# Kernel optimization log

Measured on AMD Instinct MI355X. Metric: run time of the kernel, lower is better.

Reference implementation:

```python
import jax, jax.numpy as jnp
import numpy as np
from jax import lax

CORRKS = 7
EPS_CORR = 1e-6
EPS_IN = 1e-5
FLOW_SCALE = 1.0


def _gauss_kernel2d():
    # kornia get_gaussian_kernel1d(7, 1.5), separable -> outer product
    x = np.arange(7, dtype=np.float32) - 3.0
    g = np.exp(-(x ** 2) / (2.0 * 1.5 ** 2))
    g = g / g.sum()
    return jnp.asarray(np.outer(g, g), dtype=jnp.float32)  # [7,7]


def conv2d(x, w, b=None, padding=1, dilation=1, groups=1):
    y = lax.conv_general_dilated(
        x, w, window_strides=(1, 1),
        padding=[(padding, padding), (padding, padding)],
        rhs_dilation=(dilation, dilation),
        dimension_numbers=("NCHW", "OIHW", "NCHW"),
        feature_group_count=groups)
    if b is not None:
        y = y + b[None, :, None, None]
    return y


def gaussian_blur(x):
    # replicate padding then depthwise 7x7 gaussian conv
    c = x.shape[1]
    k2 = _gauss_kernel2d()
    w = jnp.broadcast_to(k2[None, None], (c, 1, 7, 7))
    xp = jnp.pad(x, ((0, 0), (0, 0), (3, 3), (3, 3)), mode="edge")
    return conv2d(xp, w, padding=0, groups=c)


def instance_norm(x, gamma, beta):
    mu = x.mean(axis=(2, 3), keepdims=True)
    var = x.var(axis=(2, 3), keepdims=True)
    xn = (x - mu) * lax.rsqrt(var + EPS_IN)
    return xn * gamma[None, :, None, None] + beta[None, :, None, None]


def lrelu(x):
    return jnp.where(x >= 0, x, 0.2 * x)


def nan0(x):
    return jnp.nan_to_num(x, nan=0.0, posinf=0.0, neginf=0.0)


def setup_inputs() -> dict:
    key = jax.random.key(0)
    ks = jax.random.split(key, 20)
    b, c, h, w = 4, 64, 256, 256

    def rn(k, shape, scale):
        return jax.random.normal(k, shape, dtype=jnp.float32) * scale

    d = {}
    d["feat1"] = rn(ks[0], (b, c, h, w), 1.0)
    d["feat2"] = rn(ks[1], (b, c, h, w), 1.0)
    # preprocessor: Conv(c, c, 3, pad=1), bias, no norm/act
    d["pre_w"] = rn(ks[2], (c, c, 3, 3), 0.05)
    d["pre_b"] = jnp.zeros((c,), jnp.float32)
    # featcompressor layer1: Conv(2c,2c,3), IN affine + LeakyReLU (no bias)
    d["fc1_w"] = rn(ks[3], (2 * c, 2 * c, 3, 3), 0.05)
    d["fc1_g"] = jnp.ones((2 * c,), jnp.float32)
    d["fc1_be"] = jnp.zeros((2 * c,), jnp.float32)
    # featcompressor layer2: Conv(2c,c,3), bias, no norm/act
    d["fc2_w"] = rn(ks[4], (c, 2 * c, 3, 3), 0.05)
    d["fc2_b"] = jnp.zeros((c,), jnp.float32)
    # estimator: (c+49)->64 d1, 64->32 d2, 32->16 d4; IN + LeakyReLU, no bias
    d["e1_w"] = rn(ks[5], (64, c + CORRKS * CORRKS, 3, 3), 0.05)
    d["e1_g"] = jnp.ones((64,), jnp.float32)
    d["e1_be"] = jnp.zeros((64,), jnp.float32)
    d["e2_w"] = rn(ks[6], (32, 64, 3, 3), 0.05)
    d["e2_g"] = jnp.ones((32,), jnp.float32)
    d["e2_be"] = jnp.zeros((32,), jnp.float32)
    d["e3_w"] = rn(ks[7], (16, 32, 3, 3), 0.05)
    d["e3_g"] = jnp.ones((16,), jnp.float32)
    d["e3_be"] = jnp.zeros((16,), jnp.float32)
    # flow head (torch zero-inits; use small random so output is non-degenerate)
    d["head_w"] = rn(ks[8], (2, 16, 3, 3), 0.05)
    d["head_b"] = jnp.zeros((2,), jnp.float32)
    return d


def reference(feat1, feat2, pre_w, pre_b, fc1_w, fc1_g, fc1_be, fc2_w, fc2_b,
              e1_w, e1_g, e1_be, e2_w, e2_g, e2_be, e3_w, e3_g, e3_be,
              head_w, head_b):
    # preprocessor applied to both features (cat on batch == apply separately)
    f1 = conv2d(feat1, pre_w, pre_b, padding=1)
    f2 = conv2d(feat2, pre_w, pre_b, padding=1)

    # featcompressor
    feat = conv2d(jnp.concatenate([f1, f2], axis=1), fc1_w, padding=1)
    feat = lrelu(instance_norm(feat, fc1_g, fc1_be))
    feat = conv2d(feat, fc2_w, fc2_b, padding=1)

    # local correlation: (feat2 - shifted blurred feat1)^2 mean over channels
    b, c, h, w = f2.shape
    f1s = gaussian_blur(f1)
    pad = CORRKS // 2  # corr_dilation=1
    f1p = jnp.pad(f1s, ((0, 0), (0, 0), (pad, pad), (pad, pad)))  # zero pad (F.unfold)
    lc = jnp.stack(
        [((f2 - f1p[:, :, i:i + h, j:j + w]) ** 2).mean(axis=1)
         for i in range(CORRKS) for j in range(CORRKS)], axis=1)  # [b,49,h,w]
    lc = lc / (lc.mean(axis=(1, 2, 3), keepdims=True) + EPS_CORR)
    corr = nan0(jnp.concatenate([feat, lc], axis=1))  # [b, c+49, h, w]

    # dilated conv estimator stack
    x = lrelu(instance_norm(conv2d(corr, e1_w, padding=1, dilation=1), e1_g, e1_be))
    x = lrelu(instance_norm(conv2d(x, e2_w, padding=2, dilation=2), e2_g, e2_be))
    x = lrelu(instance_norm(conv2d(x, e3_w, padding=4, dilation=4), e3_g, e3_be))

    disp = conv2d(x, head_w, head_b, padding=1) * FLOW_SCALE
    disp = nan0(gaussian_blur(disp))
    return disp
```

## Files before the change

### kernel.cpp

```cpp
#include <hip/hip_runtime.h>
#include <hip/hip_bf16.h>


typedef __attribute__((ext_vector_type(8))) short short8;
typedef __attribute__((ext_vector_type(4))) float f32x4;
typedef _Float16 f16x8 __attribute__((ext_vector_type(8)));

__device__ __forceinline__ float s2f(short s) {
    unsigned int u = ((unsigned int)(unsigned short)s) << 16;
    float f; __builtin_memcpy(&f, &u, 4); return f;
}
__device__ __forceinline__ short f2s(float f) {
    __hip_bfloat16 h = __float2bfloat16(f);
    short s; __builtin_memcpy(&s, &h, 2); return s;
}
__device__ __forceinline__ short f2h(float f) {
    _Float16 h = (_Float16)f;
    short s; __builtin_memcpy(&s, &h, 2); return s;
}

__device__ __forceinline__ float gw(int j) {
    const float G[7] = {0.0366329f, 0.1112808f, 0.2167453f, 0.2706821f,
                        0.2167453f, 0.1112808f, 0.0366329f};
    return G[j];
}

__global__ __launch_bounds__(256) void transpose_k(const float* __restrict__ in,
                                                   short* __restrict__ out)
{
    __shared__ float t[64][65];
    const int b = blockIdx.y;
    const int px0 = blockIdx.x * 64;
    #pragma unroll
    for (int k = 0; k < 16; ++k) {
        int idx = threadIdx.x + k * 256;
        int c = idx >> 6, x = idx & 63;
        t[c][x] = in[(size_t)(b * 64 + c) * 65536 + px0 + x];
    }
    __syncthreads();
    #pragma unroll
    for (int k = 0; k < 16; ++k) {
        int idx = threadIdx.x + k * 256;
        int px = idx >> 6, c = idx & 63;
        out[(size_t)(b * 65536 + px0 + px) * 64 + c] = f2s(t[c][px]);
    }
}

__global__ __launch_bounds__(256) void repack2_k(const float* __restrict__ w,
                                                 short* __restrict__ o,
                                                 int cout, int cin, int CINP)
{
    int idx = blockIdx.x * 256 + threadIdx.x;
    int CB = CINP >> 5;
    int tot = cout * 9 * CINP;
    if (idx >= tot) return;
    int c8   = idx & 7;
    int lane = (idx >> 3) & 63;
    int rest = idx >> 9;
    int cb   = rest % CB;
    int rest2 = rest / CB;
    int tap  = rest2 % 9;
    int o16  = rest2 / 9;
    int n16 = lane & 15, q = lane >> 4;
    int oc = o16 * 16 + n16;
    int ic = cb * 32 + q * 8 + c8;
    float v = (ic < cin) ? w[(size_t)(oc * cin + ic) * 9 + tap] : 0.f;
    o[idx] = f2s(v);
}

template<int DIL, int CINP, int WX, int WY, int NOC, int G, int MODE>
__global__ __launch_bounds__(256) void convmfma_k(
    const short* __restrict__ srcA, const short* __restrict__ srcB,
    int splitK, int csA, int csB,
    const short* __restrict__ wgt, const float* __restrict__ bias,
    short* __restrict__ out, int OSTR, int OBASE, int b0,
    const float* __restrict__ xf)
{
    static_assert(WX * WY == 4, "4 waves per block");
    constexpr int PXW = G * 16;
    constexpr int PXB = PXW * WX;
    constexpr int XT  = 256 / PXB;
    constexpr int CB  = CINP / 32;
    constexpr int UQ  = CINP / 8;
    constexpr int LUQ = (UQ == 16) ? 4 : ((UQ == 8) ? 3 : 2);
    static_assert(UQ == (1 << LUQ), "UQ must be 4/8/16");
    constexpr int UPX = UQ + 1;
    constexpr int WPX = PXB + 2 * DIL;
    constexpr int NTOT = WPX * UQ;
    constexpr int NIT  = (NTOT + 255) / 256;

    __shared__ __align__(16) short lds[WPX * UPX * 8];

    const int tid  = threadIdx.x;
    const int lane = tid & 63;
    const int wave = tid >> 6;
    const int q = lane >> 4, n16 = lane & 15;
    const int wx = wave % WX, wy = wave / WX;

    constexpr int NX = XT * 256;
    const int bx = blockIdx.x;
    const int xs = (bx & 7) * (NX >> 3) + (bx >> 3);
    const int xt = xs % XT;
    const int y  = xs / XT;

    const int b  = b0 + blockIdx.z;
    const int ocWaveBase = blockIdx.y * (16 * NOC * WY) + wy * (16 * NOC);
    const int o16base = ocWaveBase >> 4;
    const int x0 = xt * PXB + wx * PXW;
    const int gxbase = xt * PXB - DIL;

    const int bC = b * CINP;
    const float sc = (MODE == 2) ? 1.f / (xf[b] * (1.f / 3211264.f) + 1e-6f) : 0.f;

    short8 stg[NIT];

    auto issue = [&](int yy) {
        const int rowbase = (b * 256 + yy) * 256;
        #pragma unroll
        for (int it = 0; it < NIT; ++it) {
            const int i = tid + it * 256;
            short8 v = {0, 0, 0, 0, 0, 0, 0, 0};
            if (i < NTOT) {
                const int pxl = i >> LUQ;
                const int u   = i & (UQ - 1);
                const int gx  = gxbase + pxl;
                if ((unsigned)gx < 256u) {
                    const int ic = u * 8;
                    const short* p = (ic < splitK)
                        ? srcA + (size_t)(rowbase + gx) * csA + ic
                        : srcB + (size_t)(rowbase + gx) * csB + (ic - splitK);
                    v = *reinterpret_cast<const short8*>(p);
                }
            }
            stg[it] = v;
        }
    };

    auto commit = [&]() {
        #pragma unroll
        for (int it = 0; it < NIT; ++it) {
            const int i = tid + it * 256;
            if (i < NTOT) {
                const int pxl = i >> LUQ;
                const int u   = i & (UQ - 1);
                short8 v = stg[it];
                if (MODE == 1) {
                    const int gx = gxbase + pxl;
                    if ((unsigned)gx < 256u) {
                        const int ic = u * 8;
                        #pragma unroll
                        for (int c = 0; c < 8; ++c) {
                            const float ka = xf[2 * (bC + ic + c)];
                            const float kb = xf[2 * (bC + ic + c) + 1];
                            float t = s2f(v[c]) * ka + kb;
                            t = fmaxf(t, 0.2f * t);
                            v[c] = f2s(t);
                        }
                    }
                } else if (MODE == 2) {
                    const int gx = gxbase + pxl;
                    const int ic = u * 8;
                    if ((unsigned)gx < 256u && ic >= splitK) {
                        #pragma unroll
                        for (int c = 0; c < 8; ++c)
                            v[c] = f2s(s2f(v[c]) * sc);
                    }
                }
                *reinterpret_cast<short8*>(&lds[(pxl * UPX + u) * 8]) = v;
            }
        }
    };

    f32x4 acc[G][NOC];
    #pragma unroll
    for (int g = 0; g < G; ++g)
        #pragma unroll
        for (int t = 0; t < NOC; ++t)
            acc[g][t] = {0.f, 0.f, 0.f, 0.f};

    {
        const int yy0 = y - DIL;
        if ((unsigned)yy0 < 256u) issue(yy0);
    }

    for (int dyi = 0; dyi < 3; ++dyi) {
        const int yy = y + (dyi - 1) * DIL;
        const bool rowok = ((unsigned)yy < 256u);
        __syncthreads();
        if (rowok) commit();
        __syncthreads();
        if (dyi < 2) {
            const int yn = y + dyi * DIL;
            if ((unsigned)yn < 256u) issue(yn);
        }
        if (!rowok) continue;

        #pragma unroll
        for (int dxi = 0; dxi < 3; ++dxi) {
            const int tap = dyi * 3 + dxi;
            #pragma unroll
            for (int cb = 0; cb < CB; ++cb) {
                short8 bfr[G];
                #pragma unroll
                for (int g = 0; g < G; ++g) {
                    const int pxl = wx * PXW + g * 16 + n16 + dxi * DIL;
                    bfr[g] = *reinterpret_cast<const short8*>(
                        &lds[(pxl * UPX + cb * 4 + q) * 8]);
                }
                #pragma unroll
                for (int t = 0; t < NOC; ++t) {
                    short8 a = *reinterpret_cast<const short8*>(
                        wgt + ((((size_t)(o16base + t) * 9 + tap) * CB + cb) * 64 + lane) * 8);
                    #pragma unroll
                    for (int g = 0; g < G; ++g)
                        acc[g][t] = __builtin_amdgcn_mfma_f32_16x16x32_bf16(
                            a, bfr[g], acc[g][t], 0, 0, 0);
                }
            }
        }
    }

    #pragma unroll
    for (int g = 0; g < G; ++g) {
        const size_t px_lin = (size_t)(b * 256 + y) * 256 + x0 + g * 16 + n16;
        #pragma unroll
        for (int t = 0; t < NOC; ++t) {
            const int oc = ocWaveBase + t * 16 + q * 4;
            f32x4 v = acc[g][t];
            if (bias) {
                v.x += bias[oc];     v.y += bias[oc + 1];
                v.z += bias[oc + 2]; v.w += bias[oc + 3];
            }
            ushort4 pk;
            pk.x = (unsigned short)f2s(v.x);
            pk.y = (unsigned short)f2s(v.y);
            pk.z = (unsigned short)f2s(v.z);
            pk.w = (unsigned short)f2s(v.w);
            *reinterpret_cast<ushort4*>(out + px_lin * OSTR + OBASE + oc) = pk;
        }
    }
}

__global__ __launch_bounds__(256) void in_stats_nhwc_k(const short* __restrict__ x,
                                                       float* __restrict__ sums,
                                                       int C, int lC)
{
    __shared__ float ls[256], lss[256];
    const int tid = threadIdx.x;
    const int b = blockIdx.y;
    const int c = tid & (C - 1);
    const int sub = tid >> lC;
    const int tpc = 256 >> lC;
    const int px0 = blockIdx.x * 512;
    float s = 0.f, ss = 0.f;
    for (int p = sub; p < 512; p += tpc) {
        float v = s2f(x[(size_t)(b * 65536 + px0 + p) * C + c]);
        s += v; ss += v * v;
    }
    ls[tid] = s; lss[tid] = ss;
    __syncthreads();
    if (tid < C) {
        float s0 = ls[tid], ss0 = lss[tid];
        for (int j = 1; j < tpc; ++j) { s0 += ls[tid + j * C]; ss0 += lss[tid + j * C]; }
        atomicAdd(sums + 2 * (b * C + tid), s0);
        atomicAdd(sums + 2 * (b * C + tid) + 1, ss0);
    }
}

__global__ __launch_bounds__(256) void in_finalize_k(const float* __restrict__ sums,
                                                     float* __restrict__ stats,
                                                     const float* __restrict__ gamma,
                                                     const float* __restrict__ beta,
                                                     int lC, int n)
{
    int i = blockIdx.x * 256 + threadIdx.x;
    if (i >= n) return;
    int c = i & ((1 << lC) - 1);
    float m = sums[2 * i] * (1.f / 65536.f);
    float var = sums[2 * i + 1] * (1.f / 65536.f) - m * m;
    if (var < 0.f) var = 0.f;
    float ka = rsqrtf(var + 1e-5f) * gamma[c];
    stats[2 * i] = ka;
    stats[2 * i + 1] = beta[c] - m * ka;
}

__global__ __launch_bounds__(256) void blur_k(const short* __restrict__ A,
                                              short* __restrict__ B1)
{
    __shared__ __align__(16) short raw[484 * 8];
    __shared__ __align__(16) float hb[352 * 12];

    const int tid  = threadIdx.x;
    const int tile = blockIdx.x >> 3;
    const int g    = blockIdx.x & 7;
    const int c0   = g * 8;
    const int tx = (tile & 15) << 4;
    const int ty = (tile >> 4) << 4;
    const int b  = blockIdx.y;

    #pragma unroll
    for (int it = 0; it < 2; ++it) {
        int i = tid + it * 256;
        if (i < 484) {
            int y = i / 22, x = i - y * 22;
            int gy = ty + y - 3, gx = tx + x - 3;
            gy = gy < 0 ? 0 : (gy > 255 ? 255 : gy);
            gx = gx < 0 ? 0 : (gx > 255 ? 255 : gx);
            *reinterpret_cast<short8*>(&raw[i * 8]) =
                *reinterpret_cast<const short8*>(
                    &A[(size_t)((b << 16) + (gy << 8) + gx) * 128 + c0]);
        }
    }
    __syncthreads();

    #pragma unroll
    for (int it = 0; it < 2; ++it) {
        int i = tid + it * 256;
        if (i < 352) {
            int r = i >> 4, cc = i & 15;
            float s[8];
            #pragma unroll
            for (int c = 0; c < 8; ++c) s[c] = 0.f;
            #pragma unroll
            for (int j = 0; j < 7; ++j) {
                short8 v = *reinterpret_cast<const short8*>(&raw[(r * 22 + cc + j) * 8]);
                float w = gw(j);
                #pragma unroll
                for (int c = 0; c < 8; ++c) s[c] += w * s2f(v[c]);
            }
            #pragma unroll
            for (int c = 0; c < 8; ++c) hb[i * 12 + c] = s[c];
        }
    }
    __syncthreads();

    const int py = tid >> 4, px = tid & 15;
    float s[8];
    #pragma unroll
    for (int c = 0; c < 8; ++c) s[c] = 0.f;
    #pragma unroll
    for (int j = 0; j < 7; ++j) {
        const float* hp = &hb[((py + j) * 16 + px) * 12];
        float w = gw(j);
        #pragma unroll
        for (int c = 0; c < 8; ++c) s[c] += w * hp[c];
    }
    short8 ov;
    #pragma unroll
    for (int c = 0; c < 8; ++c) ov[c] = f2h(s[c]);
    *reinterpret_cast<short8*>(
        &B1[(size_t)(((g * 4 + b) << 16) + ((ty + py) << 8) + tx + px) * 8]) = ov;
}

__global__ __launch_bounds__(256, 2) void corr2_k(const short* __restrict__ A,
                                                  const short* __restrict__ B1,
                                                  short* __restrict__ lcPad,
                                                  float* __restrict__ lcsum)
{
    __shared__ __align__(16) short blh[2][22 * 24 * 8];
    __shared__ float red[4];

    const int tid = threadIdx.x;
    const int tx = (blockIdx.x & 15) << 4;
    const int ty = (blockIdx.x >> 4) << 4;
    const int b  = blockIdx.y;
    const int py = tid >> 4, px = tid & 15;

    int y0 = tid / 22, x0c = tid - y0 * 22;
    int gy0 = ty + y0 - 3, gx0 = tx + x0c - 3;
    const bool ok0 = (gy0 >= 0 && gy0 < 256 && gx0 >= 0 && gx0 < 256);
    gy0 = gy0 < 0 ? 0 : (gy0 > 255 ? 255 : gy0);
    gx0 = gx0 < 0 ? 0 : (gx0 > 255 ? 255 : gx0);
    const int off0 = (gy0 << 8) + gx0;
    const int lc0 = y0 * 24 + x0c;

    const int c1 = tid + 256;
    int y1 = c1 / 22, x1c = c1 - y1 * 22;
    int gy1 = ty + y1 - 3, gx1 = tx + x1c - 3;
    const bool ok1 = (gy1 >= 0 && gy1 < 256 && gx1 >= 0 && gx1 < 256);
    gy1 = gy1 < 0 ? 0 : (gy1 > 255 ? 255 : gy1);
    gx1 = gx1 < 0 ? 0 : (gx1 > 255 ? 255 : gx1);
    const int off1 = (gy1 << 8) + gx1;
    const int lc1 = y1 * 24 + x1c;
    const bool has1 = (c1 < 484);

    const short* f2p = &A[(size_t)((b << 16) + ((ty + py) << 8) + tx + px) * 128 + 64];

    float acc[49];
    #pragma unroll
    for (int k = 0; k < 49; ++k) acc[k] = 0.f;

    for (int g = 0; g < 8; ++g) {
        const size_t plane = (size_t)(g * 4 + b) << 16;
        short* buf = blh[g & 1];

        {
            short8 v = *reinterpret_cast<const short8*>(&B1[(plane + off0) * 8]);
            if (!ok0) v = v ^ v;
            *reinterpret_cast<short8*>(&buf[lc0 * 8]) = v;
            if (has1) {
                short8 w = *reinterpret_cast<const short8*>(&B1[(plane + off1) * 8]);
                if (!ok1) w = w ^ w;
                *reinterpret_cast<short8*>(&buf[lc1 * 8]) = w;
            }
        }

        short8 f2raw = *reinterpret_cast<const short8*>(f2p + g * 8);
        f16x8 f2v;
        #pragma unroll
        for (int c = 0; c < 8; ++c) f2v[c] = (_Float16)s2f(f2raw[c]);

        __syncthreads();

        const short* blp = &buf[(py * 24 + px) * 8];
        #pragma unroll
        for (int i = 0; i < 7; ++i)
            #pragma unroll
            for (int j = 0; j < 7; ++j) {
                f16x8 bv = *reinterpret_cast<const f16x8*>(blp + (i * 24 + j) * 8);
                f16x8 d = f2v - bv;
                float a = acc[i * 7 + j];
#if __has_builtin(__builtin_amdgcn_fdot2)
                a = __builtin_amdgcn_fdot2(__builtin_shufflevector(d, d, 0, 1),
                                           __builtin_shufflevector(d, d, 0, 1), a, false);
                a = __builtin_amdgcn_fdot2(__builtin_shufflevector(d, d, 2, 3),
                                           __builtin_shufflevector(d, d, 2, 3), a, false);
                a = __builtin_amdgcn_fdot2(__builtin_shufflevector(d, d, 4, 5),
                                           __builtin_shufflevector(d, d, 4, 5), a, false);
                a = __builtin_amdgcn_fdot2(__builtin_shufflevector(d, d, 6, 7),
                                           __builtin_shufflevector(d, d, 6, 7), a, false);
#else
                #pragma unroll
                for (int c = 0; c < 8; ++c) {
                    float df = (float)d[c];
                    a += df * df;
                }
#endif
                acc[i * 7 + j] = a;
            }
        __syncthreads();
    }

    const size_t base = (size_t)((b << 16) + ((ty + py) << 8) + tx + px) * 64;
    float tot = 0.f;
    #pragma unroll
    for (int k = 0; k < 49; ++k) {
        float m = acc[k] * (1.f / 64.f);
        lcPad[base + k] = f2s(m);
        tot += m;
    }
    #pragma unroll
    for (int k = 49; k < 64; ++k) lcPad[base + k] = 0;

    for (int o = 32; o; o >>= 1) tot += __shfl_down(tot, o);
    if ((tid & 63) == 0) red[tid >> 6] = tot;
    __syncthreads();
    if (tid == 0) atomicAdd(lcsum + b, red[0] + red[1] + red[2] + red[3]);
}

__global__ __launch_bounds__(256) void head_k(const short* __restrict__ e3,
                                              const float* __restrict__ w,
                                              const float* __restrict__ bias,
                                              const float* __restrict__ kst,
                                              float* __restrict__ hd)
{
    int pix = blockIdx.x * 256 + threadIdx.x;
    int b = pix >> 16, rem = pix & 65535;
    int y = rem >> 8, x = rem & 255;
    float ka[16], kb[16];
    #pragma unroll
    for (int ic = 0; ic < 16; ++ic) {
        ka[ic] = kst[2 * (b * 16 + ic)];
        kb[ic] = kst[2 * (b * 16 + ic) + 1];
    }
    float a0 = bias[0], a1 = bias[1];
    #pragma unroll
    for (int tap = 0; tap < 9; ++tap) {
        int yy = y + tap / 3 - 1, xx = x + tap % 3 - 1;
        if ((unsigned)yy >= 256u || (unsigned)xx >= 256u) continue;
        const short* p = e3 + (size_t)((b << 16) + (yy << 8) + xx) * 16;
        #pragma unroll
        for (int ic = 0; ic < 16; ++ic) {
            float v = s2f(p[ic]) * ka[ic] + kb[ic];
            v = fmaxf(v, 0.2f * v);
            a0 += v * w[ic * 9 + tap];
            a1 += v * w[(16 + ic) * 9 + tap];
        }
    }
    hd[(size_t)(b * 2) * 65536 + rem]     = a0;
    hd[(size_t)(b * 2 + 1) * 65536 + rem] = a1;
}

__global__ __launch_bounds__(256) void blur7f_k(const float* __restrict__ in,
                                                float* __restrict__ out)
{
    __shared__ float raw[22 * 22];
    __shared__ float hb[22 * 16];
    const int tid = threadIdx.x;
    const int tx = (blockIdx.x & 15) << 4;
    const int ty = (blockIdx.x >> 4) << 4;
    const size_t ch = ((size_t)blockIdx.y) << 16;
    const int py = tid >> 4, px = tid & 15;

    for (int i = tid; i < 484; i += 256) {
        int y = i / 22, x = i - y * 22;
        int gy = ty + y - 3, gx = tx + x - 3;
        gy = gy < 0 ? 0 : (gy > 255 ? 255 : gy);
        gx = gx < 0 ? 0 : (gx > 255 ? 255 : gx);
        raw[i] = in[ch + (gy << 8) + gx];
    }
    __syncthreads();
    for (int i = tid; i < 352; i += 256) {
        int r = i >> 4, cc = i & 15;
        float s = 0.f;
        #pragma unroll
        for (int j = 0; j < 7; ++j) s += gw(j) * raw[r * 22 + cc + j];
        hb[i] = s;
    }
    __syncthreads();
    float s = 0.f;
    #pragma unroll
    for (int j = 0; j < 7; ++j) s += gw(j) * hb[(py + j) * 16 + px];
    out[ch + ((ty + py) << 8) + tx + px] = s;
}

extern "C" void kernel_launch(void* const* d_in, const int* in_sizes, int n_in,
                              void* d_out, int out_size, void* d_ws, size_t ws_size,
                              hipStream_t stream)
{
    const float* feat1  = (const float*)d_in[0];
    const float* feat2  = (const float*)d_in[1];
    const float* pre_w  = (const float*)d_in[2];
    const float* pre_b  = (const float*)d_in[3];
    const float* fc1_w  = (const float*)d_in[4];
    const float* fc1_g  = (const float*)d_in[5];
    const float* fc1_be = (const float*)d_in[6];
    const float* fc2_w  = (const float*)d_in[7];
    const float* fc2_b  = (const float*)d_in[8];
    const float* e1_w   = (const float*)d_in[9];
    const float* e1_g   = (const float*)d_in[10];
    const float* e1_be  = (const float*)d_in[11];
    const float* e2_w   = (const float*)d_in[12];
    const float* e2_g   = (const float*)d_in[13];
    const float* e2_be  = (const float*)d_in[14];
    const float* e3_w   = (const float*)d_in[15];
    const float* e3_g   = (const float*)d_in[16];
    const float* e3_be  = (const float*)d_in[17];
    const float* head_w = (const float*)d_in[18];
    const float* head_b = (const float*)d_in[19];
    float* out = (float*)d_out;

    const size_t NEED = 152000000;
    if (ws_size < NEED) return;

    char* ws = (char*)d_ws;
    short* T1      = (short*)(ws);
    short* T2      = (short*)(ws + 33554432);
    short* lcPad   = (short*)(ws);
    short* B1h     = (short*)(ws + 33554432);
    short* featBuf = (short*)(ws + 33554432);
    short* A       = (short*)(ws + 67108864);
    short* FC1o    = (short*)(ws + 83886080);
    short* E1o     = (short*)(ws + 67108864);
    short* E2o     = (short*)(ws + 100663296);
    short* E3o     = (short*)(ws + 117440512);
    float* HD      = (float*)(ws + 125829120);
    short* preW    = (short*)(ws + 150994944);
    short* fc1W    = (short*)(ws + 151068672);
    short* fc2W    = (short*)(ws + 151363584);
    short* e1W     = (short*)(ws + 151511040);
    short* e2W     = (short*)(ws + 151658496);
    short* e3W     = (short*)(ws + 151695360);
    float* sums0   = (float*)(ws + 151704576);
    float* sums1   = (float*)(ws + 151708672);
    float* sums2   = (float*)(ws + 151712768);
    float* sums3   = (float*)(ws + 151716864);
    float* stats0  = (float*)(ws + 151720960);
    float* stats1  = (float*)(ws + 151725056);
    float* stats2  = (float*)(ws + 151729152);
    float* stats3  = (float*)(ws + 151733248);
    float* LS      = (float*)(ws + 151737344);

    hipMemsetAsync(ws + 151704576, 0, 32784, stream);

    transpose_k<<<dim3(1024, 4), 256, 0, stream>>>(feat1, T1);
    transpose_k<<<dim3(1024, 4), 256, 0, stream>>>(feat2, T2);

    repack2_k<<<144, 256, 0, stream>>>(pre_w, preW, 64, 64, 64);
    repack2_k<<<576, 256, 0, stream>>>(fc1_w, fc1W, 128, 128, 128);
    repack2_k<<<288, 256, 0, stream>>>(fc2_w, fc2W, 64, 128, 128);
    repack2_k<<<288, 256, 0, stream>>>(e1_w, e1W, 64, 113, 128);
    repack2_k<<<72, 256, 0, stream>>>(e2_w, e2W, 32, 64, 64);
    repack2_k<<<18, 256, 0, stream>>>(e3_w, e3W, 16, 32, 32);

    convmfma_k<1, 64, 2, 2, 2, 4, 0><<<dim3(512, 1, 4), 256, 0, stream>>>(
        T1, T1, 64, 64, 64, preW, pre_b, A, 128, 0, 0, nullptr);
    convmfma_k<1, 64, 2, 2, 2, 4, 0><<<dim3(512, 1, 4), 256, 0, stream>>>(
        T2, T2, 64, 64, 64, preW, pre_b, A, 128, 64, 0, nullptr);

    blur_k<<<dim3(2048, 4), 256, 0, stream>>>(A, B1h);
    corr2_k<<<dim3(256, 4), 256, 0, stream>>>(A, B1h, lcPad, LS);

    for (int b = 3; b >= 0; --b)
        convmfma_k<1, 128, 2, 2, 4, 2, 0><<<dim3(1024, 1, 1), 256, 0, stream>>>(
            A, A, 128, 128, 128, fc1W, nullptr, FC1o, 128, 0, b, nullptr);
    in_stats_nhwc_k<<<dim3(128, 4), 256, 0, stream>>>(FC1o, sums0, 128, 7);
    in_finalize_k<<<2, 256, 0, stream>>>(sums0, stats0, fc1_g, fc1_be, 7, 512);

    convmfma_k<1, 128, 2, 2, 2, 4, 1><<<dim3(512, 1, 4), 256, 0, stream>>>(
        FC1o, FC1o, 128, 128, 128, fc2W, fc2_b, featBuf, 64, 0, 0, stats0);

    convmfma_k<1, 128, 2, 2, 2, 4, 2><<<dim3(512, 1, 4), 256, 0, stream>>>(
        featBuf, lcPad, 64, 64, 64, e1W, nullptr, E1o, 64, 0, 0, LS);
    in_stats_nhwc_k<<<dim3(128, 4), 256, 0, stream>>>(E1o, sums1, 64, 6);
    in_finalize_k<<<1, 256, 0, stream>>>(sums1, stats1, e1_g, e1_be, 6, 256);

    convmfma_k<2, 64, 2, 2, 1, 4, 1><<<dim3(512, 1, 4), 256, 0, stream>>>(
        E1o, E1o, 64, 64, 64, e2W, nullptr, E2o, 32, 0, 0, stats1);
    in_stats_nhwc_k<<<dim3(128, 4), 256, 0, stream>>>(E2o, sums2, 32, 5);
    in_finalize_k<<<1, 256, 0, stream>>>(sums2, stats2, e2_g, e2_be, 5, 128);

    convmfma_k<4, 32, 4, 1, 1, 4, 1><<<dim3(256, 1, 4), 256, 0, stream>>>(
        E2o, E2o, 32, 32, 32, e3W, nullptr, E3o, 16, 0, 0, stats2);
    in_stats_nhwc_k<<<dim3(128, 4), 256, 0, stream>>>(E3o, sums3, 16, 4);
    in_finalize_k<<<1, 256, 0, stream>>>(sums3, stats3, e3_g, e3_be, 4, 64);

    head_k<<<1024, 256, 0, stream>>>(E3o, head_w, head_b, stats3, HD);
    blur7f_k<<<dim3(256, 8), 256, 0, stream>>>(HD, out);
}
```

Baseline: 910.5 us.

## Overlap input-norm transform with MFMA taps and merge paired launches

The per-element normalize/LeakyReLU or correlation-scale transform on staged input rows moves out of the LDS commit step. It now runs on the prefetched registers in slices interleaved between the three dx taps of the MFMA loop, so the ALU work can hide behind matrix math instead of sitting between barriers. Separately, the two feature transposes are merged into one launch, and the two preprocessor convolutions are merged into one launch using a z-split that selects source and output offset. This cuts launch count and raises grid size, at the cost of more register pressure from holding transformed staging data longer.

```diff
diff --git a/kernel.cpp b/kernel.cpp
--- a/kernel.cpp
+++ b/kernel.cpp
@@ -25,11 +25,16 @@
     return G[j];
 }
 
-__global__ __launch_bounds__(256) void transpose_k(const float* __restrict__ in,
-                                                   short* __restrict__ out)
+__global__ __launch_bounds__(256) void transpose_k(const float* __restrict__ in1,
+                                                   const float* __restrict__ in2,
+                                                   short* __restrict__ out1,
+                                                   short* __restrict__ out2)
 {
     __shared__ float t[64][65];
-    const int b = blockIdx.y;
+    const int z = blockIdx.y;
+    const float* in = (z < 4) ? in1 : in2;
+    short* out = (z < 4) ? out1 : out2;
+    const int b = z & 3;
     const int px0 = blockIdx.x * 64;
     #pragma unroll
     for (int k = 0; k < 16; ++k) {
@@ -74,7 +79,7 @@
     int splitK, int csA, int csB,
     const short* __restrict__ wgt, const float* __restrict__ bias,
     short* __restrict__ out, int OSTR, int OBASE, int b0,
-    const float* __restrict__ xf)
+    const float* __restrict__ xf, int zsplit, int obDelta)
 {
     static_assert(WX * WY == 4, "4 waves per block");
     constexpr int PXW = G * 16;
@@ -103,7 +108,12 @@
     const int xt = xs % XT;
     const int y  = xs / XT;
 
-    const int b  = b0 + blockIdx.z;
+    int zz = blockIdx.z;
+    const short* s0 = srcA;
+    int obase = OBASE;
+    if (zz >= zsplit) { zz -= zsplit; s0 = srcB; obase += obDelta; }
+    const int b  = b0 + zz;
+
     const int ocWaveBase = blockIdx.y * (16 * NOC * WY) + wy * (16 * NOC);
     const int o16base = ocWaveBase >> 4;
     const int x0 = xt * PXB + wx * PXW;
@@ -127,12 +137,46 @@
                 if ((unsigned)gx < 256u) {
                     const int ic = u * 8;
                     const short* p = (ic < splitK)
-                        ? srcA + (size_t)(rowbase + gx) * csA + ic
+                        ? s0 + (size_t)(rowbase + gx) * csA + ic
                         : srcB + (size_t)(rowbase + gx) * csB + (ic - splitK);
                     v = *reinterpret_cast<const short8*>(p);
                 }
             }
             stg[it] = v;
+        }
+    };
+
+    auto transform = [&](int it0, int it1) {
+        if (MODE == 0) return;
+        #pragma unroll
+        for (int it = 0; it < NIT; ++it) {
+            if (it < it0 || it >= it1) continue;
+            const int i = tid + it * 256;
+            if (i >= NTOT) continue;
+            const int pxl = i >> LUQ;
+            const int u   = i & (UQ - 1);
+            const int gx  = gxbase + pxl;
+            if ((unsigned)gx >= 256u) continue;
+            const int ic = u * 8;
+            short8 v = stg[it];
+            if (MODE == 1) {
+                #pragma unroll
+                for (int c = 0; c < 8; ++c) {
+                    const float ka = xf[2 * (bC + ic + c)];
+                    const float kb = xf[2 * (bC + ic + c) + 1];
+                    float t = s2f(v[c]) * ka + kb;
+                    t = fmaxf(t, 0.2f * t);
+                    v[c] = f2s(t);
+                }
+                stg[it] = v;
+            } else if (MODE == 2) {
+                if (ic >= splitK) {
+                    #pragma unroll
+                    for (int c = 0; c < 8; ++c)
+                        v[c] = f2s(s2f(v[c]) * sc);
+                    stg[it] = v;
+                }
+            }
         }
     };
 
@@ -143,30 +187,7 @@
             if (i < NTOT) {
                 const int pxl = i >> LUQ;
                 const int u   = i & (UQ - 1);
-                short8 v = stg[it];
-                if (MODE == 1) {
-                    const int gx = gxbase + pxl;
-                    if ((unsigned)gx < 256u) {
-                        const int ic = u * 8;
-                        #pragma unroll
-                        for (int c = 0; c < 8; ++c) {
-                            const float ka = xf[2 * (bC + ic + c)];
-                            const float kb = xf[2 * (bC + ic + c) + 1];
-                            float t = s2f(v[c]) * ka + kb;
-                            t = fmaxf(t, 0.2f * t);
-                            v[c] = f2s(t);
-                        }
-                    }
-                } else if (MODE == 2) {
-                    const int gx = gxbase + pxl;
-                    const int ic = u * 8;
-                    if ((unsigned)gx < 256u && ic >= splitK) {
-                        #pragma unroll
-                        for (int c = 0; c < 8; ++c)
-                            v[c] = f2s(s2f(v[c]) * sc);
-                    }
-                }
-                *reinterpret_cast<short8*>(&lds[(pxl * UPX + u) * 8]) = v;
+                *reinterpret_cast<short8*>(&lds[(pxl * UPX + u) * 8]) = stg[it];
             }
         }
     };
@@ -180,7 +201,7 @@
 
     {
         const int yy0 = y - DIL;
-        if ((unsigned)yy0 < 256u) issue(yy0);
+        if ((unsigned)yy0 < 256u) { issue(yy0); transform(0, NIT); }
     }
 
     for (int dyi = 0; dyi < 3; ++dyi) {
@@ -189,34 +210,37 @@
         __syncthreads();
         if (rowok) commit();
         __syncthreads();
-        if (dyi < 2) {
-            const int yn = y + dyi * DIL;
-            if ((unsigned)yn < 256u) issue(yn);
-        }
-        if (!rowok) continue;
-
-        #pragma unroll
-        for (int dxi = 0; dxi < 3; ++dxi) {
-            const int tap = dyi * 3 + dxi;
+        const int yn = y + dyi * DIL;
+        const bool nextok = (dyi < 2) && ((unsigned)yn < 256u);
+        if (nextok) issue(yn);
+
+        if (rowok) {
             #pragma unroll
-            for (int cb = 0; cb < CB; ++cb) {
-                short8 bfr[G];
+            for (int dxi = 0; dxi < 3; ++dxi) {
+                const int tap = dyi * 3 + dxi;
                 #pragma unroll
-                for (int g = 0; g < G; ++g) {
-                    const int pxl = wx * PXW + g * 16 + n16 + dxi * DIL;
-                    bfr[g] = *reinterpret_cast<const short8*>(
-                        &lds[(pxl * UPX + cb * 4 + q) * 8]);
+                for (int cb = 0; cb < CB; ++cb) {
+                    short8 bfr[G];
+                    #pragma unroll
+                    for (int g = 0; g < G; ++g) {
+                        const int pxl = wx * PXW + g * 16 + n16 + dxi * DIL;
+                        bfr[g] = *reinterpret_cast<const short8*>(
+                            &lds[(pxl * UPX + cb * 4 + q) * 8]);
+                    }
+                    #pragma unroll
+                    for (int t = 0; t < NOC; ++t) {
+                        short8 a = *reinterpret_cast<const short8*>(
+                            wgt + ((((size_t)(o16base + t) * 9 + tap) * CB + cb) * 64 + lane) * 8);
+                        #pragma unroll
+                        for (int g = 0; g < G; ++g)
+                            acc[g][t] = __builtin_amdgcn_mfma_f32_16x16x32_bf16(
+                                a, bfr[g], acc[g][t], 0, 0, 0);
+                    }
                 }
-                #pragma unroll
-                for (int t = 0; t < NOC; ++t) {
-                    short8 a = *reinterpret_cast<const short8*>(
-                        wgt + ((((size_t)(o16base + t) * 9 + tap) * CB + cb) * 64 + lane) * 8);
-                    #pragma unroll
-                    for (int g = 0; g < G; ++g)
-                        acc[g][t] = __builtin_amdgcn_mfma_f32_16x16x32_bf16(
-                            a, bfr[g], acc[g][t], 0, 0, 0);
-                }
-            }
+                if (nextok) transform((dxi * NIT) / 3, ((dxi + 1) * NIT) / 3);
+            }
+        } else if (nextok) {
+            transform(0, NIT);
         }
     }
 
@@ -236,7 +260,7 @@
             pk.y = (unsigned short)f2s(v.y);
             pk.z = (unsigned short)f2s(v.z);
             pk.w = (unsigned short)f2s(v.w);
-            *reinterpret_cast<ushort4*>(out + px_lin * OSTR + OBASE + oc) = pk;
+            *reinterpret_cast<ushort4*>(out + px_lin * OSTR + obase + oc) = pk;
         }
     }
 }
@@ -583,8 +607,7 @@
 
     hipMemsetAsync(ws + 151704576, 0, 32784, stream);
 
-    transpose_k<<<dim3(1024, 4), 256, 0, stream>>>(feat1, T1);
-    transpose_k<<<dim3(1024, 4), 256, 0, stream>>>(feat2, T2);
+    transpose_k<<<dim3(1024, 8), 256, 0, stream>>>(feat1, feat2, T1, T2);
 
     repack2_k<<<144, 256, 0, stream>>>(pre_w, preW, 64, 64, 64);
     repack2_k<<<576, 256, 0, stream>>>(fc1_w, fc1W, 128, 128, 128);
@@ -593,35 +616,33 @@
     repack2_k<<<72, 256, 0, stream>>>(e2_w, e2W, 32, 64, 64);
     repack2_k<<<18, 256, 0, stream>>>(e3_w, e3W, 16, 32, 32);
 
-    convmfma_k<1, 64, 2, 2, 2, 4, 0><<<dim3(512, 1, 4), 256, 0, stream>>>(
-        T1, T1, 64, 64, 64, preW, pre_b, A, 128, 0, 0, nullptr);
-    convmfma_k<1, 64, 2, 2, 2, 4, 0><<<dim3(512, 1, 4), 256, 0, stream>>>(
-        T2, T2, 64, 64, 64, preW, pre_b, A, 128, 64, 0, nullptr);
+    convmfma_k<1, 64, 2, 2, 2, 4, 0><<<dim3(512, 1, 8), 256, 0, stream>>>(
+        T1, T2, 64, 64, 64, preW, pre_b, A, 128, 0, 0, nullptr, 4, 64);
 
     blur_k<<<dim3(2048, 4), 256, 0, stream>>>(A, B1h);
     corr2_k<<<dim3(256, 4), 256, 0, stream>>>(A, B1h, lcPad, LS);
 
     for (int b = 3; b >= 0; --b)
         convmfma_k<1, 128, 2, 2, 4, 2, 0><<<dim3(1024, 1, 1), 256, 0, stream>>>(
-            A, A, 128, 128, 128, fc1W, nullptr, FC1o, 128, 0, b, nullptr);
+            A, A, 128, 128, 128, fc1W, nullptr, FC1o, 128, 0, b, nullptr, 100, 0);
     in_stats_nhwc_k<<<dim3(128, 4), 256, 0, stream>>>(FC1o, sums0, 128, 7);
     in_finalize_k<<<2, 256, 0, stream>>>(sums0, stats0, fc1_g, fc1_be, 7, 512);
 
     convmfma_k<1, 128, 2, 2, 2, 4, 1><<<dim3(512, 1, 4), 256, 0, stream>>>(
-        FC1o, FC1o, 128, 128, 128, fc2W, fc2_b, featBuf, 64, 0, 0, stats0);
+        FC1o, FC1o, 128, 128, 128, fc2W, fc2_b, featBuf, 64, 0, 0, stats0, 100, 0);
 
     convmfma_k<1, 128, 2, 2, 2, 4, 2><<<dim3(512, 1, 4), 256, 0, stream>>>(
-        featBuf, lcPad, 64, 64, 64, e1W, nullptr, E1o, 64, 0, 0, LS);
+        featBuf, lcPad, 64, 64, 64, e1W, nullptr, E1o, 64, 0, 0, LS, 100, 0);
     in_stats_nhwc_k<<<dim3(128, 4), 256, 0, stream>>>(E1o, sums1, 64, 6);
     in_finalize_k<<<1, 256, 0, stream>>>(sums1, stats1, e1_g, e1_be, 6, 256);
 
     convmfma_k<2, 64, 2, 2, 1, 4, 1><<<dim3(512, 1, 4), 256, 0, stream>>>(
-        E1o, E1o, 64, 64, 64, e2W, nullptr, E2o, 32, 0, 0, stats1);
+        E1o, E1o, 64, 64, 64, e2W, nullptr, E2o, 32, 0, 0, stats1, 100, 0);
     in_stats_nhwc_k<<<dim3(128, 4), 256, 0, stream>>>(E2o, sums2, 32, 5);
     in_finalize_k<<<1, 256, 0, stream>>>(sums2, stats2, e2_g, e2_be, 5, 128);
 
     convmfma_k<4, 32, 4, 1, 1, 4, 1><<<dim3(256, 1, 4), 256, 0, stream>>>(
-        E2o, E2o, 32, 32, 32, e3W, nullptr, E3o, 16, 0, 0, stats2);
+        E2o, E2o, 32, 32, 32, e3W, nullptr, E3o, 16, 0, 0, stats2, 100, 0);
     in_stats_nhwc_k<<<dim3(128, 4), 256, 0, stream>>>(E3o, sums3, 16, 4);
     in_finalize_k<<<1, 256, 0, stream>>>(sums3, stats3, e3_g, e3_be, 4, 64);
 
```

After: 969.0 us. 1.06x slower.
